# Kernel tuning notes

Measured on AMD Instinct MI355X. Metric: run time of the kernel, lower is better.

Reference implementation:

```python
import jax, jax.numpy as jnp
import numpy as np

B, C, H, W = 4, 256, 64, 64
N = H * W


def _c1(Wt, x, b=None):
    # 1x1 conv2d: Wt [out,in], x [B,in,H,W]
    r = jnp.einsum('oi,bihw->bohw', Wt, x)
    return r if b is None else r + b[None, :, None, None]


def setup_inputs() -> dict:
    key = jax.random.key(0)
    ks = jax.random.split(key, 32)
    s = 0.01  # torch init: normal(0, 0.01)
    d = {
        'x': jax.random.normal(ks[0], (B, C, H, W), jnp.float32),
        'y': jax.random.normal(ks[1], (B, C, H, W), jnp.float32),
        'z': jax.random.normal(ks[2], (B, C, 6, 6), jnp.float32),
        'm': jax.random.normal(ks[3], (B, C, 3, 3), jnp.float32),
        'Wv':  jax.random.normal(ks[4], (C, C), jnp.float32) * s,   # conv_value, no bias
        'Wv2': jax.random.normal(ks[5], (C, C), jnp.float32) * s,   # conv_value_2, no bias
        'Wq':  jax.random.normal(ks[6], (C, C), jnp.float32) * s,
        'bq':  jnp.zeros((C,), jnp.float32),
        'Wk':  jax.random.normal(ks[7], (C, C), jnp.float32) * s,
        'bk':  jnp.zeros((C,), jnp.float32),
        'Wq2': jax.random.normal(ks[8], (C, C), jnp.float32) * s,
        'bq2': jnp.zeros((C,), jnp.float32),
        'Wk2': jax.random.normal(ks[9], (C, C), jnp.float32) * s,
        'bk2': jnp.zeros((C,), jnp.float32),
        'Win1': jax.random.normal(ks[10], (C, C), jnp.float32) * s,
        'bin1': jnp.zeros((C,), jnp.float32),
        'Win3': jax.random.normal(ks[11], (C, C), jnp.float32) * s,
        'bin3': jnp.zeros((C,), jnp.float32),
        'Wtr':  jax.random.normal(ks[12], (2 * C, 2 * C), jnp.float32) * s,
        'btr':  jnp.zeros((2 * C,), jnp.float32),
        'Wout2': jax.random.normal(ks[13], (C, C), jnp.float32) * s,
        'bout2': jnp.zeros((C,), jnp.float32),
        'Wout3': jax.random.normal(ks[14], (C, C), jnp.float32) * s,
        'bout3': jnp.zeros((C,), jnp.float32),
        'Wfc': jax.random.normal(ks[15], (36, 9), jnp.float32) * (1.0 / 3.0),  # nn.Linear(9,36)
        'bfc': jnp.zeros((36,), jnp.float32),
        # gammas init to 0 in torch, which zeroes the attention branch; use
        # nonzero values so the baseline exercises the full graph.
        'gamma':  jnp.full((1,), 0.5, jnp.float32),
        'gamma2': jnp.full((1,), 0.5, jnp.float32),
    }
    return d


def reference(x, y, z, m, Wv, Wv2, Wq, bq, Wk, bk, Wq2, bq2, Wk2, bk2,
              Win1, bin1, Win3, bin3, Wtr, btr, Wout2, bout2, Wout3, bout3,
              Wfc, bfc, gamma, gamma2):
    Bs, Cc, Hh, Ww = x.shape
    Nn = Hh * Ww
    # conv_value on y, z, m (no bias)
    yv = _c1(Wv, y)
    zv = _c1(Wv, z)
    mv = _c1(Wv, m)
    y_line = yv.reshape(Bs, Cc, Nn)            # [B,C,N]
    z_line = zv.reshape(Bs, Cc, 36)            # [B,C,36]
    m_line = mv.reshape(Bs, Cc, 9) @ Wfc.T + bfc   # [B,C,36]
    m_line = jnp.transpose(m_line, (0, 2, 1))      # [B,36,C]
    fuse_mz = jnp.einsum('bcn,bnd->bcd', z_line, m_line)      # [B,C,C]
    fuse_mzy = jnp.einsum('bcd,bdn->bcn', fuse_mz, y_line).reshape(yv.shape) + yv  # [B,C,H,W]

    value = fuse_mzy.reshape(Bs, Cc, Nn)                      # [B,C,N]
    value_2 = _c1(Wv2, x).reshape(Bs, Cc, Nn)
    query = _c1(Wq, x, bq).reshape(Bs, Cc, Nn)
    key = _c1(Wk, fuse_mzy, bk).reshape(Bs, Cc, Nn)
    query_2 = _c1(Wq2, x, bq2).reshape(Bs, Cc, Nn)
    key_2 = _c1(Wk2, x, bk2).reshape(Bs, Cc, Nn)

    # branch 1: Q^T K -> softmax over keys -> @ V^T
    sim = jax.nn.softmax(jnp.einsum('bcn,bcm->bnm', query, key), axis=2)
    out_sim = jnp.einsum('bnm,bcm->bcn', sim, value).reshape(Bs, Cc, Hh, Ww)
    out_sim = gamma[0] * out_sim

    # branch 2
    sim2 = jax.nn.softmax(jnp.einsum('bcn,bcm->bnm', query_2, key_2), axis=2)
    out_sim_2 = jnp.einsum('bnm,bcm->bcn', sim2, value_2).reshape(Bs, Cc, Hh, Ww)
    out_sim_2 = gamma2[0] * out_sim_2

    # sigmoid-gated fusion
    H_1 = _c1(Win1, out_sim, bin1)
    H_3 = _c1(Win3, out_sim_2, bin3)
    H_tra = _c1(Wtr, jnp.concatenate([H_1, H_3], axis=1), btr)
    H_5 = jax.nn.sigmoid(_c1(Wout2, H_tra[:, :Cc], bout2))
    H_6 = jax.nn.sigmoid(_c1(Wout3, H_tra[:, Cc:], bout3))
    H_all = jax.nn.softmax(jnp.stack([H_5, H_6], axis=0), axis=0)
    return H_all[0] * out_sim + H_all[1] * out_sim_2 + x
```

## Files before the change

### kernel.cpp

```cpp
#include <hip/hip_runtime.h>

typedef unsigned short u16;
typedef unsigned int   u32;
typedef int   v4i __attribute__((ext_vector_type(4)));
typedef float v4f __attribute__((ext_vector_type(4)));

__device__ __forceinline__ float b2f(u16 v) {
    union { unsigned u; float f; } t; t.u = ((unsigned)v) << 16; return t.f;
}
__device__ __forceinline__ u16 f2b(float f) {
    union { float f; unsigned u; } t; t.f = f;
    unsigned r = (t.u + 0x7FFFu + ((t.u >> 16) & 1u)) >> 16;
    return (u16)r;
}
__device__ __forceinline__ u16 f2b_trunc(float f) {
    union { float f; unsigned u; } t; t.f = f;
    return (u16)(t.u >> 16);
}
__device__ __forceinline__ v4f mfma16(v4i a, v4i b, v4f c) {
    asm("v_mfma_f32_16x16x32_bf16 %0, %1, %2, %0" : "+v"(c) : "v"(a), "v"(b));
    return c;
}
__device__ __forceinline__ void gload16(const u16* g, u16* l) {
    __builtin_amdgcn_global_load_lds(
        (const __attribute__((address_space(1))) unsigned int*)g,
        (__attribute__((address_space(3))) unsigned int*)l,
        16, 0, 0);
}

struct WCvt { const float* s[9]; u16* d[9]; int n[9]; };
__global__ void cvt_weights(WCvt p) {
    int wi = blockIdx.y;
    int i = blockIdx.x * 256 + threadIdx.x;
    if (i < p.n[wi]) p.d[wi][i] = f2b(p.s[wi][i]);
}

__global__ void cvt_t(const float* __restrict__ W1, const float* __restrict__ W3,
                      const float* __restrict__ Wv,
                      u16* __restrict__ T1, u16* __restrict__ T3, u16* __restrict__ Tv)
{
    const int zz = blockIdx.z;
    const float* src = (zz == 0) ? W1 : (zz == 1) ? W3 : Wv;
    u16* dst = (zz == 0) ? T1 : (zz == 1) ? T3 : Tv;
    __shared__ float t[32][33];
    const int r0 = blockIdx.x * 32, c0 = blockIdx.y * 32;
    const int tx = threadIdx.x, ty = threadIdx.y;
#pragma unroll
    for (int i = 0; i < 4; i++)
        t[ty + i * 8][tx] = src[(long)(r0 + ty + i * 8) * 256 + c0 + tx];
    __syncthreads();
#pragma unroll
    for (int i = 0; i < 4; i++)
        dst[(long)(c0 + ty + i * 8) * 256 + r0 + tx] = f2b(t[tx][ty + i * 8]);
}

__global__ void bias_btr(const float* __restrict__ Wtr, const float* __restrict__ bin1,
                         const float* __restrict__ bin3, const float* __restrict__ btr,
                         float* __restrict__ btr_eff)
{
    const int j = blockIdx.x, k = threadIdx.x;
    float v = Wtr[(long)j * 512 + k] * bin1[k] + Wtr[(long)j * 512 + 256 + k] * bin3[k];
    v += __shfl_xor(v, 1); v += __shfl_xor(v, 2); v += __shfl_xor(v, 4);
    v += __shfl_xor(v, 8); v += __shfl_xor(v, 16); v += __shfl_xor(v, 32);
    __shared__ float part[4];
    if ((k & 63) == 0) part[k >> 6] = v;
    __syncthreads();
    if (k == 0) btr_eff[j] = btr[j] + part[0] + part[1] + part[2] + part[3];
}

__global__ void bias_r56(const float* __restrict__ Wout2, const float* __restrict__ Wout3,
                         const float* __restrict__ bout2, const float* __restrict__ bout3,
                         const float* __restrict__ btr_eff,
                         float* __restrict__ r5, float* __restrict__ r6)
{
    const int j = blockIdx.x, k = threadIdx.x;
    float v = (j < 256) ? Wout2[(long)j * 256 + k] * btr_eff[k]
                        : Wout3[(long)(j - 256) * 256 + k] * btr_eff[256 + k];
    v += __shfl_xor(v, 1); v += __shfl_xor(v, 2); v += __shfl_xor(v, 4);
    v += __shfl_xor(v, 8); v += __shfl_xor(v, 16); v += __shfl_xor(v, 32);
    __shared__ float part[4];
    if ((k & 63) == 0) part[k >> 6] = v;
    __syncthreads();
    if (k == 0) {
        float s = part[0] + part[1] + part[2] + part[3];
        if (j < 256) r5[j] = bout2[j] + s;
        else         r6[j - 256] = bout3[j - 256] + s;
    }
}

__global__ __launch_bounds__(256) void transpose_cvt(
    const float* __restrict__ x, const float* __restrict__ y,
    u16* __restrict__ xt, u16* __restrict__ yt)
{
    const int z = blockIdx.z, t = z >> 2, b = z & 3;
    const float* src = t ? y : x;
    u16* dst = t ? yt : xt;
    __shared__ float tile[32][33];
    const int nt = blockIdx.x * 32, ct = blockIdx.y * 32;
    const int tx = threadIdx.x, ty = threadIdx.y;
#pragma unroll
    for (int i = 0; i < 4; i++)
        tile[ty + i * 8][tx] = src[((long)b * 256 + ct + ty + i * 8) * 4096 + nt + tx];
    __syncthreads();
#pragma unroll
    for (int i = 0; i < 4; i++)
        dst[((long)b * 4096 + nt + ty + i * 8) * 256 + ct + tx] = f2b(tile[tx][ty + i * 8]);
}

__global__ void small_zm(const float* __restrict__ z, const float* __restrict__ m,
                         const float* __restrict__ Wv, const float* __restrict__ Wfc,
                         const float* __restrict__ bfc,
                         float* __restrict__ zv, float* __restrict__ mline)
{
    const int o = blockIdx.x, b = blockIdx.y, tid = threadIdx.x;
    __shared__ float wrow[256];
    __shared__ float mvs[9];
    for (int i = tid; i < 256; i += 64) wrow[i] = Wv[o * 256 + i];
    __syncthreads();
    if (tid < 36) {
        float s = 0.f;
        for (int c = 0; c < 256; c++) s += wrow[c] * z[((long)b * 256 + c) * 36 + tid];
        zv[((long)b * 256 + o) * 36 + tid] = s;
    }
    if (tid < 9) {
        float s = 0.f;
        for (int c = 0; c < 256; c++) s += wrow[c] * m[((long)b * 256 + c) * 9 + tid];
        mvs[tid] = s;
    }
    __syncthreads();
    if (tid < 36) {
        float s = bfc[tid];
        for (int k = 0; k < 9; k++) s += mvs[k] * Wfc[tid * 9 + k];
        mline[((long)b * 256 + o) * 36 + tid] = s;
    }
}

__global__ void small_F(const float* __restrict__ zv, const float* __restrict__ mline,
                        u16* __restrict__ Fb, u16* __restrict__ FbT)
{
    const int c = blockIdx.x, b = blockIdx.y, d = threadIdx.x;
    const float* zr = zv + ((long)b * 256 + c) * 36;
    const float* mr = mline + ((long)b * 256 + d) * 36;
    float s = (c == d) ? 1.f : 0.f;
    for (int n = 0; n < 36; n++) s += zr[n] * mr[n];
    u16 v = f2b(s);
    Fb[((long)b * 256 + c) * 256 + d] = v;
    FbT[((long)b * 256 + d) * 256 + c] = v;
}

struct GDesc {
    const u16* X; const u16* W; const float* bias;
    u16* outT; u16* outN;
    long xbs, wbs, otbs, onbs;
    int ldx, ldw, ldot, ldon, K, rows;
};
struct GJob { GDesc d[12]; int oblk; };

__global__ __launch_bounds__(256) void gemm_tn(GJob j) {
    const int di = blockIdx.y / j.oblk;
    const int o0 = (blockIdx.y % j.oblk) * 128;
    const GDesc g = j.d[di];
    const int b = blockIdx.z;
    const int n0 = blockIdx.x * 128;
    if (n0 >= g.rows) return;
    const int tid = threadIdx.x, lane = tid & 63, w = tid >> 6;
    const int l15 = lane & 15, lg = lane >> 4;
    const int wr = (w >> 1) * 64, wc = (w & 1) * 64;

    __shared__ __align__(16) u16 As[2][4096];
    __shared__ __align__(16) u16 Bs[2][4096];

    const int sr = w * 32 + (lane >> 2);
    const int sc = (lane & 3) * 8;
    const u16* Xb_ = g.X + b * g.xbs;
    const u16* Wp_ = g.W + b * g.wbs;

    auto STAGE = [&](int buf, int ks) {
#pragma unroll
        for (int i = 0; i < 2; i++) {
            gload16(Xb_ + (long)(n0 + sr + i * 16) * g.ldx + ks * 32 + sc,
                    &As[buf][w * 1024 + i * 512]);
            gload16(Wp_ + (long)(o0 + sr + i * 16) * g.ldw + ks * 32 + sc,
                    &Bs[buf][w * 1024 + i * 512]);
        }
    };

    v4f acc[4][4];
    for (int oi = 0; oi < 4; oi++) {
        float bv = g.bias ? g.bias[o0 + wc + oi * 16 + l15] : 0.f;
        for (int mi = 0; mi < 4; mi++) acc[mi][oi] = (v4f){bv, bv, bv, bv};
    }

    const int steps = g.K >> 5;
    STAGE(0, 0);
    __syncthreads();
    for (int ks = 0; ks < steps; ks++) {
        const int cur = ks & 1;
        if (ks + 1 < steps) STAGE(cur ^ 1, ks + 1);
        v4i a[4], bb[4];
#pragma unroll
        for (int mi = 0; mi < 4; mi++)
            a[mi] = *(const v4i*)&As[cur][(wr + mi * 16 + l15) * 32 + lg * 8];
#pragma unroll
        for (int oi = 0; oi < 4; oi++)
            bb[oi] = *(const v4i*)&Bs[cur][(wc + oi * 16 + l15) * 32 + lg * 8];
#pragma unroll
        for (int mi = 0; mi < 4; mi++)
#pragma unroll
            for (int oi = 0; oi < 4; oi++)
                acc[mi][oi] = mfma16(a[mi], bb[oi], acc[mi][oi]);
        __syncthreads();
    }

    for (int mi = 0; mi < 4; mi++)
        for (int oi = 0; oi < 4; oi++) {
            int nn = n0 + wr + mi * 16 + lg * 4;
            int oo = o0 + wc + oi * 16 + l15;
            if (g.outT) {
                u16* p = g.outT + b * g.otbs + (long)nn * g.ldot + oo;
#pragma unroll
                for (int r = 0; r < 4; r++) p[(long)r * g.ldot] = f2b(acc[mi][oi][r]);
            }
            if (g.outN) {
                ushort4 pk;
                pk.x = f2b(acc[mi][oi][0]); pk.y = f2b(acc[mi][oi][1]);
                pk.z = f2b(acc[mi][oi][2]); pk.w = f2b(acc[mi][oi][3]);
                *(ushort4*)(g.outN + b * g.onbs + (long)oo * g.ldon + nn) = pk;
            }
        }
}

__global__ __launch_bounds__(256) void attn_kernel(
    const u16* __restrict__ qtA, const u16* __restrict__ ktA, const u16* __restrict__ vA,
    u16* __restrict__ otA, u16* __restrict__ onA, const float* __restrict__ gA,
    const u16* __restrict__ qtB, const u16* __restrict__ ktB, const u16* __restrict__ vB,
    u16* __restrict__ otB, u16* __restrict__ onB, const float* __restrict__ gB)
{
    const int wg = blockIdx.x;
    const int qb = wg >> 3, code = wg & 7;
    const int br = code & 1, b = code >> 1;
    const u16* Qt = br ? qtB : qtA;
    const u16* Kt = br ? ktB : ktA;
    const u16* V  = br ? vB  : vA;
    u16* Ot = br ? otB : otA;
    u16* On = br ? onB : onA;
    const float gamma = br ? gB[0] : gA[0];
    const long bs = (long)4096 * 256;
    const u16* Qb = Qt + b * bs;
    const u16* Kb = Kt + b * bs;
    const u16* Vb = V + b * bs;
    u16* Otb = Ot + b * bs;
    u16* Onb = On + b * bs;

    const int tid = threadIdx.x, lane = tid & 63, w = tid >> 6;
    const int l15 = lane & 15, lg = lane >> 4;

    __shared__ __align__(16) u16 Ksh[4][8192];
    __shared__ __align__(16) u16 P[2][64][56];
    __shared__ float den[64];

    v4i qf[8];
    const u16* qp = Qb + (long)(qb * 64 + w * 16 + l15) * 256 + lg * 8;
#pragma unroll
    for (int ks = 0; ks < 8; ks++) qf[ks] = *(const v4i*)(qp + ks * 32);

    v4f oacc[4][4];
    for (int ci = 0; ci < 4; ci++)
        for (int qi = 0; qi < 4; qi++) oacc[ci][qi] = (v4f){0.f, 0.f, 0.f, 0.f};
    float dacc[4] = {0.f, 0.f, 0.f, 0.f};

    const u16* vb = Vb + (long)(w * 64 + l15) * 4096 + lg * 8;
    v4i vfA[4], vfB[4];

    const int srow = w * 8 + (lane >> 5);
    const int scolB = (lane & 31) * 16;

    auto STAGE = [&](int buf, int t) {
        const u16* base = Kb + (long)t * 8192;
        u16* lb = &Ksh[buf][w * 2048];
#pragma unroll
        for (int i = 0; i < 4; i++) {
            int row = srow + i * 2;
            int colB = scolB ^ ((row & 7) << 4);
            gload16(base + row * 256 + (colB >> 1), lb + i * 512);
        }
    };
    auto VLOAD = [&](v4i (&vf)[4], int t) {
#pragma unroll
        for (int ci = 0; ci < 4; ci++)
            vf[ci] = *(const v4i*)(vb + (long)ci * 16 * 4096 + t * 32);
    };

    STAGE(0, 0);
    STAGE(1, 1);
    STAGE(2, 2);
    VLOAD(vfA, 0);
    asm volatile("s_waitcnt vmcnt(12)" ::: "memory");
    __builtin_amdgcn_s_barrier();
    __builtin_amdgcn_sched_barrier(0);

    auto ITER = [&](int mb, v4i (&vcur)[4], v4i (&vnxt)[4]) {
        const u16* kb = &Ksh[mb & 3][0];
        u16* Pc = &P[mb & 1][0][0];

        v4f l0a = {0,0,0,0}, l0b = {0,0,0,0}, l1a = {0,0,0,0}, l1b = {0,0,0,0};
        __builtin_amdgcn_s_setprio(1);
#pragma unroll
        for (int ks = 0; ks < 4; ks++) {
            int c0 = (ks * 64 + lg * 16) ^ ((l15 & 7) << 4);
            v4i k0 = *(const v4i*)(kb + l15 * 256 + (c0 >> 1));
            v4i k1 = *(const v4i*)(kb + (16 + l15) * 256 + (c0 >> 1));
            l0a = mfma16(qf[ks], k0, l0a);
            l1a = mfma16(qf[ks], k1, l1a);
        }
#pragma unroll
        for (int ks = 4; ks < 8; ks++) {
            int c0 = (ks * 64 + lg * 16) ^ ((l15 & 7) << 4);
            v4i k0 = *(const v4i*)(kb + l15 * 256 + (c0 >> 1));
            v4i k1 = *(const v4i*)(kb + (16 + l15) * 256 + (c0 >> 1));
            l0b = mfma16(qf[ks], k0, l0b);
            l1b = mfma16(qf[ks], k1, l1b);
        }
        __builtin_amdgcn_s_setprio(0);
        v4f lacc0 = l0a + l0b, lacc1 = l1a + l1b;

#pragma unroll
        for (int r = 0; r < 4; r++) {
            float e0 = __expf(lacc0[r]);
            float e1 = __expf(lacc1[r]);
            dacc[r] += e0 + e1;
            Pc[(w * 16 + lg * 4 + r) * 56 + l15]      = f2b_trunc(e0);
            Pc[(w * 16 + lg * 4 + r) * 56 + 16 + l15] = f2b_trunc(e1);
        }

        if (mb < 127) VLOAD(vnxt, mb + 1);
        if (mb < 125) STAGE((mb + 3) & 3, mb + 3);

        if (mb <= 124)      asm volatile("s_waitcnt vmcnt(12) lgkmcnt(0)" ::: "memory");
        else if (mb == 125) asm volatile("s_waitcnt vmcnt(8) lgkmcnt(0)" ::: "memory");
        else if (mb == 126) asm volatile("s_waitcnt vmcnt(4) lgkmcnt(0)" ::: "memory");
        else                asm volatile("s_waitcnt vmcnt(0) lgkmcnt(0)" ::: "memory");
        __builtin_amdgcn_s_barrier();
        __builtin_amdgcn_sched_barrier(0);

        v4i pf[4];
#pragma unroll
        for (int qi = 0; qi < 4; qi++)
            pf[qi] = *(const v4i*)(Pc + (qi * 16 + l15) * 56 + lg * 8);
        __builtin_amdgcn_s_setprio(1);
#pragma unroll
        for (int ci = 0; ci < 4; ci++)
#pragma unroll
            for (int qi = 0; qi < 4; qi++)
                oacc[ci][qi] = mfma16(vcur[ci], pf[qi], oacc[ci][qi]);
        __builtin_amdgcn_s_setprio(0);
    };

    for (int mb2 = 0; mb2 < 64; ++mb2) {
        ITER(2 * mb2,     vfA, vfB);
        ITER(2 * mb2 + 1, vfB, vfA);
    }

#pragma unroll
    for (int r = 0; r < 4; r++) {
        float s = dacc[r];
        s += __shfl_xor(s, 1); s += __shfl_xor(s, 2);
        s += __shfl_xor(s, 4); s += __shfl_xor(s, 8);
        if (l15 == 0) den[w * 16 + lg * 4 + r] = s;
    }
    __syncthreads();

    for (int qi = 0; qi < 4; qi++) {
        int q = qi * 16 + l15;
        float sc = gamma / den[q];
        int n = qb * 64 + q;
        for (int ci = 0; ci < 4; ci++) {
            int c0 = w * 64 + ci * 16 + lg * 4;
            ushort4 pk;
            pk.x = f2b(oacc[ci][qi][0] * sc);
            pk.y = f2b(oacc[ci][qi][1] * sc);
            pk.z = f2b(oacc[ci][qi][2] * sc);
            pk.w = f2b(oacc[ci][qi][3] * sc);
            *(ushort4*)(Otb + (long)n * 256 + c0) = pk;
            Onb[(long)(c0 + 0) * 4096 + n] = pk.x;
            Onb[(long)(c0 + 1) * 4096 + n] = pk.y;
            Onb[(long)(c0 + 2) * 4096 + n] = pk.z;
            Onb[(long)(c0 + 3) * 4096 + n] = pk.w;
        }
    }
}

__global__ __launch_bounds__(256) void gate2_gemm(
    const u16* __restrict__ Ot, const u16* __restrict__ O2t,
    const u16* __restrict__ PQ, const float* __restrict__ r5, const float* __restrict__ r6,
    const u16* __restrict__ On, const u16* __restrict__ O2n,
    const float* __restrict__ x, float* __restrict__ out)
{
    const int bz = blockIdx.z;
    const int n0 = blockIdx.x * 64, c0 = blockIdx.y * 64;
    const int tid = threadIdx.x, lane = tid & 63, w = tid >> 6;
    const int l15 = lane & 15, lg = lane >> 4;
    const int wcc = (w >> 1) * 32, wnn = (w & 1) * 32;
    const long NC = 4096L * 256;
    const long arow = c0 + wcc + l15;
    const u16* pa5 = PQ + arow * 256 + lg * 8;
    const u16* qa5 = PQ + 65536 + arow * 256 + lg * 8;
    const u16* pa6 = PQ + 131072 + arow * 256 + lg * 8;
    const u16* qa6 = PQ + 196608 + arow * 256 + lg * 8;
    const u16* bo  = Ot  + bz * NC + (long)(n0 + wnn + l15) * 256 + lg * 8;
    const u16* bo2 = O2t + bz * NC + (long)(n0 + wnn + l15) * 256 + lg * 8;

    v4f a5[2][2], a6[2][2];
    for (int mi = 0; mi < 2; mi++)
        for (int oi = 0; oi < 2; oi++) {
            a5[mi][oi] = (v4f){0, 0, 0, 0};
            a6[mi][oi] = (v4f){0, 0, 0, 0};
        }
#pragma unroll 4
    for (int k = 0; k < 256; k += 32) {
        v4i bb[2], w5[2], w6[2];
#pragma unroll
        for (int oi = 0; oi < 2; oi++) bb[oi] = *(const v4i*)(bo + (long)oi * 16 * 256 + k);
#pragma unroll
        for (int mi = 0; mi < 2; mi++) {
            w5[mi] = *(const v4i*)(pa5 + (long)mi * 16 * 256 + k);
            w6[mi] = *(const v4i*)(pa6 + (long)mi * 16 * 256 + k);
        }
#pragma unroll
        for (int mi = 0; mi < 2; mi++)
#pragma unroll
            for (int oi = 0; oi < 2; oi++) {
                a5[mi][oi] = mfma16(w5[mi], bb[oi], a5[mi][oi]);
                a6[mi][oi] = mfma16(w6[mi], bb[oi], a6[mi][oi]);
            }
    }
#pragma unroll 4
    for (int k = 0; k < 256; k += 32) {
        v4i bb[2], w5[2], w6[2];
#pragma unroll
        for (int oi = 0; oi < 2; oi++) bb[oi] = *(const v4i*)(bo2 + (long)oi * 16 * 256 + k);
#pragma unroll
        for (int mi = 0; mi < 2; mi++) {
            w5[mi] = *(const v4i*)(qa5 + (long)mi * 16 * 256 + k);
            w6[mi] = *(const v4i*)(qa6 + (long)mi * 16 * 256 + k);
        }
#pragma unroll
        for (int mi = 0; mi < 2; mi++)
#pragma unroll
            for (int oi = 0; oi < 2; oi++) {
                a5[mi][oi] = mfma16(w5[mi], bb[oi], a5[mi][oi]);
                a6[mi][oi] = mfma16(w6[mi], bb[oi], a6[mi][oi]);
            }
    }
    for (int mi = 0; mi < 2; mi++) {
        float r5v[4], r6v[4];
#pragma unroll
        for (int r = 0; r < 4; r++) {
            int c = c0 + wcc + mi * 16 + lg * 4 + r;
            r5v[r] = r5[c]; r6v[r] = r6[c];
        }
        for (int oi = 0; oi < 2; oi++) {
            int n = n0 + wnn + oi * 16 + l15;
#pragma unroll
            for (int r = 0; r < 4; r++) {
                int c = c0 + wcc + mi * 16 + lg * 4 + r;
                long base = bz * NC + (long)c * 4096 + n;
                float ov  = b2f(On[base]);
                float ov2 = b2f(O2n[base]);
                float xv  = x[((long)bz * 256 + c) * 4096 + n];
                float s5 = 1.f / (1.f + __expf(-(a5[mi][oi][r] + r5v[r])));
                float s6 = 1.f / (1.f + __expf(-(a6[mi][oi][r] + r6v[r])));
                float w0 = 1.f / (1.f + __expf(s6 - s5));
                out[((long)bz * 256 + c) * 4096 + n] = w0 * ov + (1.f - w0) * ov2 + xv;
            }
        }
    }
}

extern "C" void kernel_launch(void* const* d_in, const int* in_sizes, int n_in,
                              void* d_out, int out_size, void* d_ws, size_t ws_size,
                              hipStream_t stream)
{
    const float* x     = (const float*)d_in[0];
    const float* y     = (const float*)d_in[1];
    const float* z     = (const float*)d_in[2];
    const float* m     = (const float*)d_in[3];
    const float* Wv    = (const float*)d_in[4];
    const float* Wv2   = (const float*)d_in[5];
    const float* Wq    = (const float*)d_in[6];
    const float* bq    = (const float*)d_in[7];
    const float* Wk    = (const float*)d_in[8];
    const float* bk    = (const float*)d_in[9];
    const float* Wq2   = (const float*)d_in[10];
    const float* bq2   = (const float*)d_in[11];
    const float* Wk2   = (const float*)d_in[12];
    const float* bk2   = (const float*)d_in[13];
    const float* Win1  = (const float*)d_in[14];
    const float* bin1  = (const float*)d_in[15];
    const float* Win3  = (const float*)d_in[16];
    const float* bin3  = (const float*)d_in[17];
    const float* Wtr   = (const float*)d_in[18];
    const float* btr   = (const float*)d_in[19];
    const float* Wout2 = (const float*)d_in[20];
    const float* bout2 = (const float*)d_in[21];
    const float* Wout3 = (const float*)d_in[22];
    const float* bout3 = (const float*)d_in[23];
    const float* Wfc   = (const float*)d_in[24];
    const float* bfc   = (const float*)d_in[25];
    const float* gamma  = (const float*)d_in[26];
    const float* gamma2 = (const float*)d_in[27];

    char* ws = (char*)d_ws;
    u16* Wb[6];
    for (int i = 0; i < 6; i++) Wb[i] = (u16*)(ws + (size_t)i * 131072);
    u16* Wout2b = (u16*)(ws + 786432);
    u16* Wout3b = (u16*)(ws + 917504);
    u16* Win1T  = (u16*)(ws + 1048576);
    u16* Win3T  = (u16*)(ws + 1179648);
    u16* Fb   = (u16*)(ws + 1310720);
    u16* FbT  = (u16*)(ws + 1835008);
    u16* Gk   = (u16*)(ws + 2359296);
    u16* PQ   = (u16*)(ws + 2883584);
    u16* Tt   = (u16*)(ws + 3407872);
    float* btr_eff = (float*)(ws + 3932160);
    float* r5 = (float*)(ws + 3934208);
    float* r6 = (float*)(ws + 3935232);
    auto SLOT = [&](int i) { return ws + 4194304 + (size_t)i * 8388608; };
    u16* xt  = (u16*)SLOT(0);
    u16* yt  = (u16*)SLOT(1);
    u16* fmn = (u16*)SLOT(4);
    u16* v2n = (u16*)SLOT(5);
    u16* qt  = (u16*)SLOT(6);
    u16* kt  = (u16*)SLOT(7);
    u16* q2t = (u16*)SLOT(8);
    u16* k2t = (u16*)SLOT(9);
    u16* O2n = (u16*)SLOT(0);
    u16* Ot_ = (u16*)SLOT(1);
    u16* On_ = (u16*)SLOT(2);
    u16* O2t = (u16*)SLOT(3);
    u16* Wtrb   = (u16*)SLOT(3);
    float* zv    = (float*)(SLOT(3) + 524288);
    float* mline = (float*)(SLOT(3) + 671744);
    u16* Gv   = (u16*)(SLOT(3) + 1048576);
    u16* Gk2  = (u16*)(SLOT(3) + 1572864);
    u16* WvT  = (u16*)(SLOT(3) + 2097152);

    const long NC = 4096L * 256, CC = 65536;

    {
        WCvt wc;
        const float* wsrc[9] = {Wv, Wv2, Wq, Wk, Wq2, Wk2, Wout2, Wout3, Wtr};
        u16* wdst[9] = {Wb[0], Wb[1], Wb[2], Wb[3], Wb[4], Wb[5], Wout2b, Wout3b, Wtrb};
        for (int i = 0; i < 9; i++) { wc.s[i] = wsrc[i]; wc.d[i] = wdst[i]; wc.n[i] = (i == 8) ? 262144 : 65536; }
        cvt_weights<<<dim3(1024, 9), 256, 0, stream>>>(wc);
    }
    cvt_t<<<dim3(8, 8, 3), dim3(32, 8), 0, stream>>>(Win1, Win3, Wv, Win1T, Win3T, WvT);

    bias_btr<<<512, 256, 0, stream>>>(Wtr, bin1, bin3, btr, btr_eff);
    bias_r56<<<512, 256, 0, stream>>>(Wout2, Wout3, bout2, bout3, btr_eff, r5, r6);

    transpose_cvt<<<dim3(128, 8, 8), dim3(32, 8), 0, stream>>>(x, y, xt, yt);

    small_zm<<<dim3(256, 4), 64, 0, stream>>>(z, m, Wv, Wfc, bfc, zv, mline);
    small_F<<<dim3(256, 4), 256, 0, stream>>>(zv, mline, Fb, FbT);

    auto mkdesc = [](const u16* X, int ldx, long xbs, const u16* W, int ldw, long wbs,
                     const float* bias, u16* outT, int ldot, long otbs,
                     u16* outN, int ldon, long onbs, int K, int rows) {
        GDesc g; g.X = X; g.W = W; g.bias = bias; g.outT = outT; g.outN = outN;
        g.xbs = xbs; g.wbs = wbs; g.otbs = otbs; g.onbs = onbs;
        g.ldx = ldx; g.ldw = ldw; g.ldot = ldot; g.ldon = ldon; g.K = K; g.rows = rows;
        return g;
    };

    {
        GJob j{}; j.oblk = 2;
        j.d[0] = mkdesc(Fb, 256, CC, WvT, 256, 0, nullptr, Gv, 256, CC, nullptr, 0, 0, 256, 256);
        j.d[1] = mkdesc(Wb[3], 256, 0, FbT, 256, CC, nullptr, Gk, 256, CC, nullptr, 0, 0, 256, 256);
        for (int yy = 0; yy < 4; yy++) {
            const u16* Xw = Wtrb + ((yy >> 1) ? 131072 : 0) + ((yy & 1) ? 256 : 0);
            const u16* Ww = (yy & 1) ? Win3T : Win1T;
            j.d[2 + yy] = mkdesc(Xw, 512, 0, Ww, 256, 0, nullptr,
                                 nullptr, 0, 0, Tt + yy * 65536, 256, 0, 256, 256);
        }
        gemm_tn<<<dim3(2, 12, 4), 256, 0, stream>>>(j);
    }
    {
        GJob j{}; j.oblk = 2;
        j.d[0] = mkdesc(Gk, 256, CC, WvT, 256, 0, nullptr, Gk2, 256, CC, nullptr, 0, 0, 256, 256);
        for (int yy = 0; yy < 4; yy++) {
            const u16* Xw = (yy >> 1) ? Wout3b : Wout2b;
            j.d[1 + yy] = mkdesc(Xw, 256, 0, Tt + yy * 65536, 256, 0, nullptr,
                                 PQ + yy * 65536, 256, 0, nullptr, 0, 0, 256, 256);
        }
        gemm_tn<<<dim3(2, 10, 4), 256, 0, stream>>>(j);
    }
    {
        GJob j{}; j.oblk = 2;
        j.d[0] = mkdesc(xt, 256, NC, Wb[2], 256, 0, bq,  qt,  256, NC, nullptr, 0, 0, 256, 4096);
        j.d[1] = mkdesc(xt, 256, NC, Wb[4], 256, 0, bq2, q2t, 256, NC, nullptr, 0, 0, 256, 4096);
        j.d[2] = mkdesc(xt, 256, NC, Wb[5], 256, 0, bk2, k2t, 256, NC, nullptr, 0, 0, 256, 4096);
        j.d[3] = mkdesc(xt, 256, NC, Wb[1], 256, 0, nullptr, nullptr, 0, 0, v2n, 4096, NC, 256, 4096);
        j.d[4] = mkdesc(yt, 256, NC, Gv,  256, CC, nullptr, nullptr, 0, 0, fmn, 4096, NC, 256, 4096);
        j.d[5] = mkdesc(yt, 256, NC, Gk2, 256, CC, bk, kt, 256, NC, nullptr, 0, 0, 256, 4096);
        gemm_tn<<<dim3(32, 12, 4), 256, 0, stream>>>(j);
    }

    attn_kernel<<<dim3(512), 256, 0, stream>>>(qt, kt, fmn, Ot_, On_, gamma,
                                               q2t, k2t, v2n, O2t, O2n, gamma2);

    gate2_gemm<<<dim3(64, 4, 4), 256, 0, stream>>>(Ot_, O2t, PQ, r5, r6,
                                                   On_, O2n, x, (float*)d_out);
}
```

Measured before the change: 326.3 us.

## Fuse query projections into attention kernel prologue

Each attention workgroup now computes its own 64-row Q tile from x and the query weights with MFMA, stages it through shared memory, and loads it into fragments. This drops the two query outputs from the batched projection GEMM and avoids writing Q to global memory and reading it back. Output buffers are remapped to slots that are now free. The cost is extra per-block compute in the attention prologue, plus strided weight loads read directly from global memory without LDS reuse.

```diff
diff --git a/kernel.cpp b/kernel.cpp
--- a/kernel.cpp
+++ b/kernel.cpp
@@ -231,22 +231,25 @@
 }
 
 __global__ __launch_bounds__(256) void attn_kernel(
-    const u16* __restrict__ qtA, const u16* __restrict__ ktA, const u16* __restrict__ vA,
+    const u16* __restrict__ xt,
+    const u16* __restrict__ WqA, const float* __restrict__ bqA,
+    const u16* __restrict__ WqB, const float* __restrict__ bqB,
+    const u16* __restrict__ ktA, const u16* __restrict__ vA,
     u16* __restrict__ otA, u16* __restrict__ onA, const float* __restrict__ gA,
-    const u16* __restrict__ qtB, const u16* __restrict__ ktB, const u16* __restrict__ vB,
+    const u16* __restrict__ ktB, const u16* __restrict__ vB,
     u16* __restrict__ otB, u16* __restrict__ onB, const float* __restrict__ gB)
 {
     const int wg = blockIdx.x;
     const int qb = wg >> 3, code = wg & 7;
     const int br = code & 1, b = code >> 1;
-    const u16* Qt = br ? qtB : qtA;
     const u16* Kt = br ? ktB : ktA;
     const u16* V  = br ? vB  : vA;
     u16* Ot = br ? otB : otA;
     u16* On = br ? onB : onA;
+    const u16* Wq = br ? WqB : WqA;
+    const float* bq = br ? bqB : bqA;
     const float gamma = br ? gB[0] : gA[0];
     const long bs = (long)4096 * 256;
-    const u16* Qb = Qt + b * bs;
     const u16* Kb = Kt + b * bs;
     const u16* Vb = V + b * bs;
     u16* Otb = Ot + b * bs;
@@ -259,10 +262,39 @@
     __shared__ __align__(16) u16 P[2][64][56];
     __shared__ float den[64];
 
+    u16* Qs = &Ksh[0][0];
+    {
+        v4f qacc[16];
+#pragma unroll
+        for (int ci = 0; ci < 16; ci++) {
+            float bv = bq[ci * 16 + l15];
+            qacc[ci] = (v4f){bv, bv, bv, bv};
+        }
+        const u16* xa = xt + b * bs + (long)(qb * 64 + w * 16 + l15) * 256 + lg * 8;
+        const u16* wqp = Wq + (long)l15 * 256 + lg * 8;
+#pragma unroll
+        for (int ks = 0; ks < 8; ks++) {
+            v4i af = *(const v4i*)(xa + ks * 32);
+#pragma unroll
+            for (int ci = 0; ci < 16; ci++) {
+                v4i bf = *(const v4i*)(wqp + (long)ci * 16 * 256 + ks * 32);
+                qacc[ci] = mfma16(af, bf, qacc[ci]);
+            }
+        }
+#pragma unroll
+        for (int ci = 0; ci < 16; ci++)
+#pragma unroll
+            for (int r = 0; r < 4; r++)
+                Qs[(w * 16 + lg * 4 + r) * 264 + ci * 16 + l15] = f2b(qacc[ci][r]);
+    }
+    __syncthreads();
     v4i qf[8];
-    const u16* qp = Qb + (long)(qb * 64 + w * 16 + l15) * 256 + lg * 8;
-#pragma unroll
-    for (int ks = 0; ks < 8; ks++) qf[ks] = *(const v4i*)(qp + ks * 32);
+#pragma unroll
+    for (int ks = 0; ks < 8; ks++)
+        qf[ks] = *(const v4i*)(Qs + (long)(w * 16 + l15) * 264 + ks * 32 + lg * 8);
+    asm volatile("s_waitcnt lgkmcnt(0)" ::: "memory");
+    __builtin_amdgcn_s_barrier();
+    __builtin_amdgcn_sched_barrier(0);
 
     v4f oacc[4][4];
     for (int ci = 0; ci < 4; ci++)
@@ -530,12 +562,10 @@
     u16* yt  = (u16*)SLOT(1);
     u16* fmn = (u16*)SLOT(4);
     u16* v2n = (u16*)SLOT(5);
-    u16* qt  = (u16*)SLOT(6);
     u16* kt  = (u16*)SLOT(7);
-    u16* q2t = (u16*)SLOT(8);
     u16* k2t = (u16*)SLOT(9);
-    u16* O2n = (u16*)SLOT(0);
-    u16* Ot_ = (u16*)SLOT(1);
+    u16* Ot_ = (u16*)SLOT(6);
+    u16* O2n = (u16*)SLOT(8);
     u16* On_ = (u16*)SLOT(2);
     u16* O2t = (u16*)SLOT(3);
     u16* Wtrb   = (u16*)SLOT(3);
@@ -597,17 +627,16 @@
     }
     {
         GJob j{}; j.oblk = 2;
-        j.d[0] = mkdesc(xt, 256, NC, Wb[2], 256, 0, bq,  qt,  256, NC, nullptr, 0, 0, 256, 4096);
-        j.d[1] = mkdesc(xt, 256, NC, Wb[4], 256, 0, bq2, q2t, 256, NC, nullptr, 0, 0, 256, 4096);
-        j.d[2] = mkdesc(xt, 256, NC, Wb[5], 256, 0, bk2, k2t, 256, NC, nullptr, 0, 0, 256, 4096);
-        j.d[3] = mkdesc(xt, 256, NC, Wb[1], 256, 0, nullptr, nullptr, 0, 0, v2n, 4096, NC, 256, 4096);
-        j.d[4] = mkdesc(yt, 256, NC, Gv,  256, CC, nullptr, nullptr, 0, 0, fmn, 4096, NC, 256, 4096);
-        j.d[5] = mkdesc(yt, 256, NC, Gk2, 256, CC, bk, kt, 256, NC, nullptr, 0, 0, 256, 4096);
-        gemm_tn<<<dim3(32, 12, 4), 256, 0, stream>>>(j);
-    }
-
-    attn_kernel<<<dim3(512), 256, 0, stream>>>(qt, kt, fmn, Ot_, On_, gamma,
-                                               q2t, k2t, v2n, O2t, O2n, gamma2);
+        j.d[0] = mkdesc(xt, 256, NC, Wb[5], 256, 0, bk2, k2t, 256, NC, nullptr, 0, 0, 256, 4096);
+        j.d[1] = mkdesc(xt, 256, NC, Wb[1], 256, 0, nullptr, nullptr, 0, 0, v2n, 4096, NC, 256, 4096);
+        j.d[2] = mkdesc(yt, 256, NC, Gv,  256, CC, nullptr, nullptr, 0, 0, fmn, 4096, NC, 256, 4096);
+        j.d[3] = mkdesc(yt, 256, NC, Gk2, 256, CC, bk, kt, 256, NC, nullptr, 0, 0, 256, 4096);
+        gemm_tn<<<dim3(32, 8, 4), 256, 0, stream>>>(j);
+    }
+
+    attn_kernel<<<dim3(512), 256, 0, stream>>>(xt, Wb[2], bq, Wb[4], bq2,
+                                               kt, fmn, Ot_, On_, gamma,
+                                               k2t, v2n, O2t, O2n, gamma2);
 
     gate2_gemm<<<dim3(64, 4, 4), 256, 0, stream>>>(Ot_, O2t, PQ, r5, r6,
                                                    On_, O2n, x, (float*)d_out);
```

Result: slower. 351.6 us (+7.8%).
